# Optimization experiments

Measured on AMD Instinct MI355X. Metric: run time of the kernel, lower is better.

Reference implementation:

```python
import jax, jax.numpy as jnp
import numpy as np

N_EMBED = 1024
N_HEAD = 16
EPS = 1.1920929e-07  # torch.finfo(float32).eps, nn.RMSNorm default eps=None


def rmsnorm(x, w):
    var = jnp.mean(x * x, axis=-1, keepdims=True)
    return x * jax.lax.rsqrt(var + EPS) * w


def setup_inputs() -> dict:
    key = jax.random.key(0)
    ks = jax.random.split(key, 12)
    d = N_EMBED
    s = lambda fan_in: 1.0 / np.sqrt(fan_in)
    inp = {
        "x": jax.random.normal(ks[0], (2, 2048, d), jnp.float32),
        "w_attn": jax.random.uniform(ks[1], (d, 3 * d), jnp.float32, -s(d), s(d)),
        "b_attn": jax.random.uniform(ks[2], (3 * d,), jnp.float32, -s(d), s(d)),
        "w_proj": jax.random.uniform(ks[3], (d, d), jnp.float32, -s(d), s(d)),
        "b_proj": jax.random.uniform(ks[4], (d,), jnp.float32, -s(d), s(d)),
        "w_fc1": jax.random.uniform(ks[5], (d, 4 * d), jnp.float32, -s(d), s(d)),
        "b_fc1": jax.random.uniform(ks[6], (4 * d,), jnp.float32, -s(d), s(d)),
        "w_fc2": jax.random.uniform(ks[7], (4 * d, d), jnp.float32, -s(4 * d), s(4 * d)),
        "b_fc2": jax.random.uniform(ks[8], (d,), jnp.float32, -s(4 * d), s(4 * d)),
        "g_norm1": jnp.ones((d,), jnp.float32),
        "g_norm2": jnp.ones((d,), jnp.float32),
    }
    return inp


def reference(x, w_attn, b_attn, w_proj, b_proj, w_fc1, b_fc1, w_fc2, b_fc2, g_norm1, g_norm2):
    B, T, d = x.shape
    H = N_HEAD
    hd = d // H

    # --- attention branch ---
    h = rmsnorm(x, g_norm1)
    qkv = h @ w_attn + b_attn  # [B,T,3d]
    q, k, v = jnp.split(qkv, 3, axis=-1)
    q = q.reshape(B, T, H, hd).transpose(0, 2, 1, 3)  # [B,H,T,hd]
    k = k.reshape(B, T, H, hd).transpose(0, 2, 1, 3)
    v = v.reshape(B, T, H, hd).transpose(0, 2, 1, 3)
    qk = jnp.einsum('bhqd,bhkd->bhqk', q, k)  # NOTE: no logit scaling (as in source)
    mask = jnp.tril(jnp.ones((T, T), bool))
    qk = jnp.where(mask, qk, -jnp.inf)
    # source scales softmax OUTPUT by n_embed**-0.5 (faithful quirk)
    attn = jax.nn.softmax(qk, axis=-1) * (d ** -0.5)
    o = jnp.einsum('bhqk,bhkd->bhqd', attn, v)
    o = o.transpose(0, 2, 1, 3).reshape(B, T, d)
    x = x + (o @ w_proj + b_proj)

    # --- MLP branch ---
    h = rmsnorm(x, g_norm2)
    h = jax.nn.gelu(h @ w_fc1 + b_fc1, approximate=False)
    x = x + (h @ w_fc2 + b_fc2)
    return x
```

## Files before the change

kernel.cpp:

```cpp
#include <hip/hip_runtime.h>
#include <hip/hip_bf16.h>


typedef __hip_bfloat16 bf16;
typedef __attribute__((ext_vector_type(8))) short short8;
typedef __attribute__((ext_vector_type(4))) float floatx4;

__device__ __forceinline__ float bits2f(unsigned short u) {
  union { unsigned int i; float f; } c; c.i = ((unsigned int)u) << 16; return c.f;
}
__device__ __forceinline__ unsigned short f2bits(float f) {
  bf16 b = __float2bfloat16(f);
  union { bf16 b; unsigned short u; } c; c.b = b; return c.u;
}

__device__ __forceinline__ void gld_lds16(const unsigned short* g, unsigned short* l) {
  __builtin_amdgcn_global_load_lds(
      (const __attribute__((address_space(1))) void*)g,
      (__attribute__((address_space(3))) void*)l, 16, 0, 0);
}

__global__ __launch_bounds__(256) void rmsnorm_r10(const float* __restrict__ x,
                                                   const float* __restrict__ g,
                                                   unsigned short* __restrict__ out)
{
  const int row = blockIdx.x, tid = threadIdx.x;
  const size_t rb = (size_t)row * 1024;
  float4 xv = *(const float4*)(x + rb + tid * 4);
  float v[4] = {xv.x, xv.y, xv.z, xv.w};
  float s = v[0]*v[0] + v[1]*v[1] + v[2]*v[2] + v[3]*v[3];
  #pragma unroll
  for (int off = 32; off > 0; off >>= 1) s += __shfl_down(s, off, 64);
  __shared__ float part[4];
  if ((tid & 63) == 0) part[tid >> 6] = s;
  __syncthreads();
  const float tot = part[0] + part[1] + part[2] + part[3];
  const float sc = rsqrtf(tot * (1.0f / 1024.0f) + 1.1920929e-07f);
  float4 gv = *(const float4*)(g + tid * 4);
  ushort4 o4 = { f2bits(v[0] * sc * gv.x), f2bits(v[1] * sc * gv.y),
                 f2bits(v[2] * sc * gv.z), f2bits(v[3] * sc * gv.w) };
  *(ushort4*)(out + rb + tid * 4) = o4;
}

__global__ __launch_bounds__(256) void wprep_r10(const float* __restrict__ in,
                                                 unsigned short* __restrict__ out,
                                                 int K, int N)
{
  __shared__ unsigned short tile[32][33];
  const int tid = threadIdx.x;
  const int k0 = blockIdx.y * 32, n0 = blockIdx.x * 32;
  const int tr = tid >> 3, tc4 = (tid & 7) * 4;
  float4 v = *(const float4*)(in + (size_t)(k0 + tr) * N + n0 + tc4);
  tile[tr][tc4 + 0] = f2bits(v.x);
  tile[tr][tc4 + 1] = f2bits(v.y);
  tile[tr][tc4 + 2] = f2bits(v.z);
  tile[tr][tc4 + 3] = f2bits(v.w);
  __syncthreads();
  ushort4 o = { tile[tc4 + 0][tr], tile[tc4 + 1][tr],
                tile[tc4 + 2][tr], tile[tc4 + 3][tr] };
  *(ushort4*)(out + (size_t)(n0 + tr) * K + k0 + tc4) = o;
}

template<int EPI>
__global__ __launch_bounds__(256) void gemm_r10(
    const unsigned short* __restrict__ A,
    const unsigned short* __restrict__ BT,
    const float* __restrict__ bias,
    const float* __restrict__ resid,
    void* __restrict__ Cout,
    int M, int N, int K, int Klen)
{
  __shared__ __align__(16) unsigned short As[2][128 * 32];
  __shared__ __align__(16) unsigned short Bs[2][128 * 32];
  const int tid = threadIdx.x;
  const int lane = tid & 63;
  const int wv = tid >> 6;
  const int m0 = blockIdx.y * 128, n0 = blockIdx.x * 128;
  const int wm = (wv >> 1) * 64, wn = (wv & 1) * 64;
  const int kbase = blockIdx.z * Klen;

  const int s0 = tid, s1 = tid + 256;
  const int r0 = s0 >> 2, kq0 = (s0 & 3) ^ ((r0 >> 1) & 3);
  const int r1 = s1 >> 2, kq1 = (s1 & 3) ^ ((r1 >> 1) & 3);
  const unsigned short* Ab = A  + (size_t)m0 * K;
  const unsigned short* Bb = BT + (size_t)n0 * K;
  const size_t ga0 = (size_t)r0 * K + kq0 * 8 + kbase;
  const size_t ga1 = (size_t)r1 * K + kq1 * 8 + kbase;

  floatx4 acc[4][4];
  #pragma unroll
  for (int i = 0; i < 4; ++i)
    #pragma unroll
    for (int j = 0; j < 4; ++j)
      acc[i][j] = (floatx4){0.f, 0.f, 0.f, 0.f};

  int aoff[4], boff[4];
  #pragma unroll
  for (int i = 0; i < 4; ++i) {
    int ra = wm + i * 16 + (lane & 15);
    aoff[i] = (ra * 4 + ((lane >> 4) ^ ((ra >> 1) & 3))) * 8;
    int rb = wn + i * 16 + (lane & 15);
    boff[i] = (rb * 4 + ((lane >> 4) ^ ((rb >> 1) & 3))) * 8;
  }

  gld_lds16(Ab + ga0, As[0] + s0 * 8);
  gld_lds16(Ab + ga1, As[0] + s1 * 8);
  gld_lds16(Bb + ga0, Bs[0] + s0 * 8);
  gld_lds16(Bb + ga1, Bs[0] + s1 * 8);
  __syncthreads();

  const int nsteps = Klen >> 5;
  for (int t = 0; t < nsteps; ++t) {
    const int cur = t & 1;
    if (t + 1 < nsteps) {
      const size_t ko = (size_t)(t + 1) * 32;
      gld_lds16(Ab + ga0 + ko, As[cur ^ 1] + s0 * 8);
      gld_lds16(Ab + ga1 + ko, As[cur ^ 1] + s1 * 8);
      gld_lds16(Bb + ga0 + ko, Bs[cur ^ 1] + s0 * 8);
      gld_lds16(Bb + ga1 + ko, Bs[cur ^ 1] + s1 * 8);
    }

    short8 af[4], bfr[4];
    #pragma unroll
    for (int i = 0; i < 4; ++i) {
      af[i]  = *(const short8*)(As[cur] + aoff[i]);
      bfr[i] = *(const short8*)(Bs[cur] + boff[i]);
    }
    #pragma unroll
    for (int i = 0; i < 4; ++i)
      #pragma unroll
      for (int j = 0; j < 4; ++j)
        acc[i][j] = __builtin_amdgcn_mfma_f32_16x16x32_bf16(af[i], bfr[j], acc[i][j], 0, 0, 0);

    __syncthreads();
  }

  float* Cp32 = (float*)Cout;
  if constexpr (EPI == 4) Cp32 += (size_t)blockIdx.z * ((size_t)M * N);

  #pragma unroll
  for (int i = 0; i < 4; ++i) {
    #pragma unroll
    for (int j = 0; j < 4; ++j) {
      const int rbase = m0 + wm + i * 16 + (lane >> 4) * 4;
      const int c = n0 + wn + j * 16 + (lane & 15);
      float bia = 0.0f;
      if constexpr (EPI != 4) bia = bias[c];
      #pragma unroll
      for (int r = 0; r < 4; ++r) {
        float v = acc[i][j][r] + bia;
        const size_t idx = (size_t)(rbase + r) * N + c;
        if constexpr (EPI == 0) {
          ((unsigned short*)Cout)[idx] = f2bits(v);
        } else if constexpr (EPI == 1) {
          ((float*)Cout)[idx] = v + resid[idx];
        } else if constexpr (EPI == 2) {
          v = 0.5f * v * (1.0f + erff(v * 0.70710678118654752f));
          ((unsigned short*)Cout)[idx] = f2bits(v);
        } else if constexpr (EPI == 3) {
          ((float*)Cout)[idx] = v + resid[idx];
        } else {
          Cp32[idx] = v;
        }
      }
    }
  }
}

__global__ __launch_bounds__(256) void red2_r10(const float* __restrict__ P,
                                                const float* __restrict__ resid,
                                                const float* __restrict__ bias,
                                                float* __restrict__ out)
{
  const size_t i = ((size_t)blockIdx.x * 256 + threadIdx.x) * 4;
  const int col = (int)(i & 1023);
  float4 p0 = *(const float4*)(P + i);
  float4 p1 = *(const float4*)(P + ((size_t)4096 * 1024) + i);
  float4 xr = *(const float4*)(resid + i);
  float4 b  = *(const float4*)(bias + col);
  float4 o  = { p0.x + p1.x + xr.x + b.x, p0.y + p1.y + xr.y + b.y,
                p0.z + p1.z + xr.z + b.z, p0.w + p1.w + xr.w + b.w };
  *(float4*)(out + i) = o;
}

__global__ __launch_bounds__(512) void attn_r10(const unsigned short* __restrict__ qkv,
                                                unsigned short* __restrict__ o)
{
  __shared__ __align__(16) unsigned short Qs[128 * 64];
  __shared__ __align__(16) unsigned short Ks[2][64 * 64];
  __shared__ __align__(16) unsigned short VT[2][64 * 72];
  __shared__ __align__(16) unsigned short Ps[128 * 72];
  __shared__ __align__(16) float stat_s[128];

  const int tid = threadIdx.x, lane = tid & 63, wv = tid >> 6;
  const int quad = lane >> 4, l15 = lane & 15;
  const int qt0 = blockIdx.x, bh = blockIdx.y;
  const int b = bh >> 4, h = bh & 15;
  const size_t base = (size_t)b * 2048 * 3072;
  const int qcol = h * 64, kcol = 1024 + h * 64, vcol = 2048 + h * 64;

  const int sr = tid >> 3, scp = tid & 7, sc = scp ^ (sr & 7);
  const unsigned short* kgp = qkv + base + (size_t)sr * 3072 + kcol + sc * 8;
  const int vp = tid & 31, vdc = tid >> 5;
  const unsigned short* vgp = qkv + base + (size_t)(2 * vp) * 3072 + vcol + vdc * 4;

  for (int pass = 0; pass < 2; ++pass) {
    const int qt = pass ? qt0 : 15 - qt0;
    const int q0 = qt * 128;
    const int nkt = 2 * qt + 2;

    __syncthreads();

    #pragma unroll
    for (int p = 0; p < 2; ++p) {
      int s = tid + 512 * p;
      int r = s >> 3, cp = s & 7, c = cp ^ (r & 7);
      gld_lds16(qkv + base + (size_t)(q0 + r) * 3072 + qcol + c * 8, Qs + s * 8);
    }
    gld_lds16(kgp, Ks[0] + tid * 8);
    {
      uint2 u0 = *(const uint2*)vgp;
      uint2 u1 = *(const uint2*)(vgp + 3072);
      unsigned short* dst = VT[0] + (size_t)(vdc * 4) * 72 + 2 * vp;
      *(unsigned int*)(dst + 0 * 72) = (u0.x & 0xffffu) | (u1.x << 16);
      *(unsigned int*)(dst + 1 * 72) = (u0.x >> 16)     | (u1.x & 0xffff0000u);
      *(unsigned int*)(dst + 2 * 72) = (u0.y & 0xffffu) | (u1.y << 16);
      *(unsigned int*)(dst + 3 * 72) = (u0.y >> 16)     | (u1.y & 0xffff0000u);
    }
    __syncthreads();

    short8 qa[2];
    #pragma unroll
    for (int ks = 0; ks < 2; ++ks) {
      int ra = wv * 16 + l15;
      int cp = (ks * 4 + quad) ^ (ra & 7);
      qa[ks] = *(const short8*)(Qs + (ra * 8 + cp) * 8);
    }

    floatx4 oacc[4];
    #pragma unroll
    for (int dt = 0; dt < 4; ++dt) oacc[dt] = (floatx4){0.f, 0.f, 0.f, 0.f};
    float m_i[4], l_i[4];
    #pragma unroll
    for (int r = 0; r < 4; ++r) { m_i[r] = -3.0e38f; l_i[r] = 0.0f; }

    for (int kt = 0; kt < nkt; ++kt) {
      const int cur = kt & 1;
      const bool pf = (kt + 1 < nkt);
      uint2 u0, u1;
      if (pf) {
        const size_t koff = (size_t)(kt + 1) * 64 * 3072;
        gld_lds16(kgp + koff, Ks[cur ^ 1] + tid * 8);
        u0 = *(const uint2*)(vgp + koff);
        u1 = *(const uint2*)(vgp + koff + 3072);
      }

      short8 kb[4][2];
      #pragma unroll
      for (int j = 0; j < 4; ++j)
        #pragma unroll
        for (int ks = 0; ks < 2; ++ks) {
          int rb = j * 16 + l15;
          int cp = (ks * 4 + quad) ^ (rb & 7);
          kb[j][ks] = *(const short8*)(Ks[cur] + (rb * 8 + cp) * 8);
        }
      floatx4 s_[4];
      #pragma unroll
      for (int j = 0; j < 4; ++j) s_[j] = (floatx4){0.f, 0.f, 0.f, 0.f};
      #pragma unroll
      for (int j = 0; j < 4; ++j)
        #pragma unroll
        for (int ks = 0; ks < 2; ++ks)
          s_[j] = __builtin_amdgcn_mfma_f32_16x16x32_bf16(qa[ks], kb[j][ks], s_[j], 0, 0, 0);

      const int k0 = kt * 64;
      const int rowmin = q0 + wv * 16;
      const int rowb = rowmin + quad * 4;
      if (k0 + 63 > rowmin) {
        #pragma unroll
        for (int j = 0; j < 4; ++j) {
          const int col = k0 + j * 16 + l15;
          #pragma unroll
          for (int r = 0; r < 4; ++r)
            if (col > rowb + r) s_[j][r] = -3.0e38f;
        }
      }
      float fm[4], al[4], rs[4];
      #pragma unroll
      for (int r = 0; r < 4; ++r)
        fm[r] = fmaxf(fmaxf(s_[0][r], s_[1][r]), fmaxf(s_[2][r], s_[3][r]));
      #pragma unroll
      for (int msk = 1; msk < 16; msk <<= 1)
        #pragma unroll
        for (int r = 0; r < 4; ++r)
          fm[r] = fmaxf(fm[r], __shfl_xor(fm[r], msk, 64));
      #pragma unroll
      for (int r = 0; r < 4; ++r) {
        const float mn = fmaxf(m_i[r], fm[r]);
        al[r] = __expf(m_i[r] - mn);
        m_i[r] = mn;
      }
      #pragma unroll
      for (int j = 0; j < 4; ++j)
        #pragma unroll
        for (int r = 0; r < 4; ++r)
          s_[j][r] = __expf(s_[j][r] - m_i[r]);
      #pragma unroll
      for (int r = 0; r < 4; ++r)
        rs[r] = (s_[0][r] + s_[1][r]) + (s_[2][r] + s_[3][r]);
      #pragma unroll
      for (int msk = 1; msk < 16; msk <<= 1)
        #pragma unroll
        for (int r = 0; r < 4; ++r)
          rs[r] += __shfl_xor(rs[r], msk, 64);
      #pragma unroll
      for (int r = 0; r < 4; ++r)
        l_i[r] = l_i[r] * al[r] + rs[r];
      if (l15 == 0) {
        float4 a4 = { al[0], al[1], al[2], al[3] };
        *(float4*)(stat_s + wv * 16 + quad * 4) = a4;
      }
      #pragma unroll
      for (int j = 0; j < 4; ++j)
        #pragma unroll
        for (int r = 0; r < 4; ++r)
          Ps[(size_t)(wv * 16 + quad * 4 + r) * 72 + j * 16 + l15] = f2bits(s_[j][r]);

      const float alq = stat_s[wv * 16 + l15];
      #pragma unroll
      for (int dt = 0; dt < 4; ++dt)
        #pragma unroll
        for (int r = 0; r < 4; ++r)
          oacc[dt][r] *= alq;

      short8 va[4][2], pb[2];
      #pragma unroll
      for (int dt = 0; dt < 4; ++dt)
        #pragma unroll
        for (int ks = 0; ks < 2; ++ks)
          va[dt][ks] = *(const short8*)(VT[cur] + (size_t)(dt * 16 + l15) * 72 + ks * 32 + quad * 8);
      #pragma unroll
      for (int ks = 0; ks < 2; ++ks)
        pb[ks] = *(const short8*)(Ps + (size_t)(wv * 16 + l15) * 72 + ks * 32 + quad * 8);
      #pragma unroll
      for (int dt = 0; dt < 4; ++dt)
        #pragma unroll
        for (int ks = 0; ks < 2; ++ks)
          oacc[dt] = __builtin_amdgcn_mfma_f32_16x16x32_bf16(va[dt][ks], pb[ks], oacc[dt], 0, 0, 0);

      if (pf) {
        unsigned short* dst = VT[cur ^ 1] + (size_t)(vdc * 4) * 72 + 2 * vp;
        *(unsigned int*)(dst + 0 * 72) = (u0.x & 0xffffu) | (u1.x << 16);
        *(unsigned int*)(dst + 1 * 72) = (u0.x >> 16)     | (u1.x & 0xffff0000u);
        *(unsigned int*)(dst + 2 * 72) = (u0.y & 0xffffu) | (u1.y << 16);
        *(unsigned int*)(dst + 3 * 72) = (u0.y >> 16)     | (u1.y & 0xffff0000u);
      }
      __syncthreads();
    }

    if (l15 == 0) {
      float4 l4 = { l_i[0], l_i[1], l_i[2], l_i[3] };
      *(float4*)(stat_s + wv * 16 + quad * 4) = l4;
    }
    const float linv = 0.03125f / stat_s[wv * 16 + l15];
    const size_t row = (size_t)b * 2048 + q0 + wv * 16 + l15;
    #pragma unroll
    for (int dt = 0; dt < 4; ++dt) {
      const int col = h * 64 + dt * 16 + quad * 4;
      ushort4 o4 = { f2bits(oacc[dt][0] * linv), f2bits(oacc[dt][1] * linv),
                     f2bits(oacc[dt][2] * linv), f2bits(oacc[dt][3] * linv) };
      *(ushort4*)(o + row * 1024 + col) = o4;
    }
  }
}

extern "C" void kernel_launch(void* const* d_in, const int* in_sizes, int n_in,
                              void* d_out, int out_size, void* d_ws, size_t ws_size,
                              hipStream_t stream)
{
  (void)in_sizes; (void)n_in; (void)out_size; (void)ws_size;
  const float* x      = (const float*)d_in[0];
  const float* w_attn = (const float*)d_in[1];
  const float* b_attn = (const float*)d_in[2];
  const float* w_proj = (const float*)d_in[3];
  const float* b_proj = (const float*)d_in[4];
  const float* w_fc1  = (const float*)d_in[5];
  const float* b_fc1  = (const float*)d_in[6];
  const float* w_fc2  = (const float*)d_in[7];
  const float* b_fc2  = (const float*)d_in[8];
  const float* g1     = (const float*)d_in[9];
  const float* g2     = (const float*)d_in[10];
  float* out = (float*)d_out;

  char* ws = (char*)d_ws;
  unsigned short* h   = (unsigned short*)(ws);
  unsigned short* qkv = (unsigned short*)(ws + ((size_t)8  << 20));
  unsigned short* ov  = (unsigned short*)(ws);
  float*          x1  = (float*)         (ws + ((size_t)32 << 20));
  unsigned short* h2  = (unsigned short*)(ws + ((size_t)8  << 20));
  unsigned short* h3  = (unsigned short*)(ws + ((size_t)48 << 20));
  unsigned short* WT  = (unsigned short*)(ws + ((size_t)80 << 20));
  float*          P   = (float*)(ws);

  const int M = 4096;

  rmsnorm_r10<<<M, 256, 0, stream>>>(x, g1, h);
  wprep_r10<<<dim3(3072 / 32, 1024 / 32), 256, 0, stream>>>(w_attn, WT, 1024, 3072);
  gemm_r10<0><<<dim3(3072 / 128, M / 128), 256, 0, stream>>>(h, WT, b_attn, nullptr, qkv, M, 3072, 1024, 1024);
  attn_r10<<<dim3(8, 32), 512, 0, stream>>>(qkv, ov);
  wprep_r10<<<dim3(1024 / 32, 1024 / 32), 256, 0, stream>>>(w_proj, WT, 1024, 1024);
  gemm_r10<1><<<dim3(1024 / 128, M / 128), 256, 0, stream>>>(ov, WT, b_proj, x, x1, M, 1024, 1024, 1024);
  rmsnorm_r10<<<M, 256, 0, stream>>>(x1, g2, h2);
  wprep_r10<<<dim3(4096 / 32, 1024 / 32), 256, 0, stream>>>(w_fc1, WT, 1024, 4096);
  gemm_r10<2><<<dim3(4096 / 128, M / 128), 256, 0, stream>>>(h2, WT, b_fc1, nullptr, h3, M, 4096, 1024, 1024);
  wprep_r10<<<dim3(1024 / 32, 4096 / 32), 256, 0, stream>>>(w_fc2, WT, 4096, 1024);
  gemm_r10<4><<<dim3(1024 / 128, M / 128, 2), 256, 0, stream>>>(h3, WT, nullptr, nullptr, P, M, 1024, 4096, 2048);
  red2_r10<<<4096, 256, 0, stream>>>(P, x1, b_fc2, out);
}
```

Before: 386.5 us.

## Add 256x256-tile GEMM with 4-stage LDS pipeline for QKV and FC1

Adds a new GEMM kernel that uses 512 threads, 256x256 output tiles, and a 4-buffer LDS ring that prefetches two K-steps ahead. The QKV and FC1 projections now use it instead of the 128x128 kernel. Larger tiles raise arithmetic intensity and reduce global traffic per FLOP, and the deeper prefetch hides load latency. In exchange, the block count drops: QKV gets 192 blocks and FC1 gets 256 on a 256-CU device, so wave quantization and lower occupancy from 64KB+ of LDS are risks.

```diff
diff --git a/kernel.cpp b/kernel.cpp
--- a/kernel.cpp
+++ b/kernel.cpp
@@ -20,7 +20,7 @@
       (__attribute__((address_space(3))) void*)l, 16, 0, 0);
 }
 
-__global__ __launch_bounds__(256) void rmsnorm_r10(const float* __restrict__ x,
+__global__ __launch_bounds__(256) void rmsnorm_r15(const float* __restrict__ x,
                                                    const float* __restrict__ g,
                                                    unsigned short* __restrict__ out)
 {
@@ -42,7 +42,7 @@
   *(ushort4*)(out + rb + tid * 4) = o4;
 }
 
-__global__ __launch_bounds__(256) void wprep_r10(const float* __restrict__ in,
+__global__ __launch_bounds__(256) void wprep_r15(const float* __restrict__ in,
                                                  unsigned short* __restrict__ out,
                                                  int K, int N)
 {
@@ -62,7 +62,7 @@
 }
 
 template<int EPI>
-__global__ __launch_bounds__(256) void gemm_r10(
+__global__ __launch_bounds__(256) void gemm128_r15(
     const unsigned short* __restrict__ A,
     const unsigned short* __restrict__ BT,
     const float* __restrict__ bias,
@@ -167,7 +167,112 @@
   }
 }
 
-__global__ __launch_bounds__(256) void red2_r10(const float* __restrict__ P,
+template<int EPI>
+__global__ __launch_bounds__(512) void gemm256_r15(
+    const unsigned short* __restrict__ A,
+    const unsigned short* __restrict__ BT,
+    const float* __restrict__ bias,
+    void* __restrict__ Cout,
+    int M, int N, int K)
+{
+  __shared__ __align__(16) unsigned short As[4][256 * 32];
+  __shared__ __align__(16) unsigned short Bs[4][256 * 32];
+  const int tid = threadIdx.x;
+  const int lane = tid & 63, wv = tid >> 6;
+  const int quad = lane >> 4, l15 = lane & 15;
+  const int m0 = blockIdx.y * 256, n0 = blockIdx.x * 256;
+  const int wm = (wv >> 2) * 128, wn = (wv & 3) * 64;
+
+  const int s0 = tid, s1 = tid + 512;
+  const int r0 = s0 >> 2, kq0 = (s0 & 3) ^ ((r0 >> 1) & 3);
+  const int r1 = s1 >> 2, kq1 = (s1 & 3) ^ ((r1 >> 1) & 3);
+  const unsigned short* Ab = A  + (size_t)m0 * K;
+  const unsigned short* Bb = BT + (size_t)n0 * K;
+  const size_t ga0 = (size_t)r0 * K + kq0 * 8;
+  const size_t ga1 = (size_t)r1 * K + kq1 * 8;
+
+  floatx4 acc[8][4];
+  #pragma unroll
+  for (int i = 0; i < 8; ++i)
+    #pragma unroll
+    for (int j = 0; j < 4; ++j)
+      acc[i][j] = (floatx4){0.f, 0.f, 0.f, 0.f};
+
+  int aoff[8], boff[4];
+  #pragma unroll
+  for (int i = 0; i < 8; ++i) {
+    int ra = wm + i * 16 + l15;
+    aoff[i] = (ra * 4 + (quad ^ ((ra >> 1) & 3))) * 8;
+  }
+  #pragma unroll
+  for (int j = 0; j < 4; ++j) {
+    int rb = wn + j * 16 + l15;
+    boff[j] = (rb * 4 + (quad ^ ((rb >> 1) & 3))) * 8;
+  }
+
+  #define STG_R15(t) { const size_t ko = (size_t)(t) * 32; const int bb = (t) & 3; \
+    gld_lds16(Ab + ga0 + ko, As[bb] + s0 * 8); \
+    gld_lds16(Ab + ga1 + ko, As[bb] + s1 * 8); \
+    gld_lds16(Bb + ga0 + ko, Bs[bb] + s0 * 8); \
+    gld_lds16(Bb + ga1 + ko, Bs[bb] + s1 * 8); }
+
+  STG_R15(0);
+  STG_R15(1);
+
+  const int nsteps = K >> 5;
+  for (int t = 0; t < nsteps; ++t) {
+    const int cur = t & 3;
+    if (t + 2 < nsteps) {
+      STG_R15(t + 2);
+      asm volatile("s_waitcnt vmcnt(8)" ::: "memory");
+    } else if (t + 1 < nsteps) {
+      asm volatile("s_waitcnt vmcnt(4)" ::: "memory");
+    } else {
+      asm volatile("s_waitcnt vmcnt(0)" ::: "memory");
+    }
+    __builtin_amdgcn_s_barrier();
+    asm volatile("" ::: "memory");
+
+    short8 bfr[4];
+    #pragma unroll
+    for (int j = 0; j < 4; ++j)
+      bfr[j] = *(const short8*)(Bs[cur] + boff[j]);
+    #pragma unroll
+    for (int ih = 0; ih < 2; ++ih) {
+      short8 af[4];
+      #pragma unroll
+      for (int k = 0; k < 4; ++k)
+        af[k] = *(const short8*)(As[cur] + aoff[ih * 4 + k]);
+      #pragma unroll
+      for (int k = 0; k < 4; ++k)
+        #pragma unroll
+        for (int j = 0; j < 4; ++j)
+          acc[ih * 4 + k][j] = __builtin_amdgcn_mfma_f32_16x16x32_bf16(af[k], bfr[j], acc[ih * 4 + k][j], 0, 0, 0);
+    }
+  }
+  #undef STG_R15
+
+  #pragma unroll
+  for (int i = 0; i < 8; ++i) {
+    #pragma unroll
+    for (int j = 0; j < 4; ++j) {
+      const int rbase = m0 + wm + i * 16 + quad * 4;
+      const int c = n0 + wn + j * 16 + l15;
+      const float bia = bias[c];
+      #pragma unroll
+      for (int r = 0; r < 4; ++r) {
+        float v = acc[i][j][r] + bia;
+        const size_t idx = (size_t)(rbase + r) * N + c;
+        if constexpr (EPI == 2) {
+          v = 0.5f * v * (1.0f + erff(v * 0.70710678118654752f));
+        }
+        ((unsigned short*)Cout)[idx] = f2bits(v);
+      }
+    }
+  }
+}
+
+__global__ __launch_bounds__(256) void red2_r15(const float* __restrict__ P,
                                                 const float* __restrict__ resid,
                                                 const float* __restrict__ bias,
                                                 float* __restrict__ out)
@@ -183,7 +288,7 @@
   *(float4*)(out + i) = o;
 }
 
-__global__ __launch_bounds__(512) void attn_r10(const unsigned short* __restrict__ qkv,
+__global__ __launch_bounds__(512) void attn_r15(const unsigned short* __restrict__ qkv,
                                                 unsigned short* __restrict__ o)
 {
   __shared__ __align__(16) unsigned short Qs[128 * 64];
@@ -404,16 +509,16 @@
 
   const int M = 4096;
 
-  rmsnorm_r10<<<M, 256, 0, stream>>>(x, g1, h);
-  wprep_r10<<<dim3(3072 / 32, 1024 / 32), 256, 0, stream>>>(w_attn, WT, 1024, 3072);
-  gemm_r10<0><<<dim3(3072 / 128, M / 128), 256, 0, stream>>>(h, WT, b_attn, nullptr, qkv, M, 3072, 1024, 1024);
-  attn_r10<<<dim3(8, 32), 512, 0, stream>>>(qkv, ov);
-  wprep_r10<<<dim3(1024 / 32, 1024 / 32), 256, 0, stream>>>(w_proj, WT, 1024, 1024);
-  gemm_r10<1><<<dim3(1024 / 128, M / 128), 256, 0, stream>>>(ov, WT, b_proj, x, x1, M, 1024, 1024, 1024);
-  rmsnorm_r10<<<M, 256, 0, stream>>>(x1, g2, h2);
-  wprep_r10<<<dim3(4096 / 32, 1024 / 32), 256, 0, stream>>>(w_fc1, WT, 1024, 4096);
-  gemm_r10<2><<<dim3(4096 / 128, M / 128), 256, 0, stream>>>(h2, WT, b_fc1, nullptr, h3, M, 4096, 1024, 1024);
-  wprep_r10<<<dim3(1024 / 32, 4096 / 32), 256, 0, stream>>>(w_fc2, WT, 4096, 1024);
-  gemm_r10<4><<<dim3(1024 / 128, M / 128, 2), 256, 0, stream>>>(h3, WT, nullptr, nullptr, P, M, 1024, 4096, 2048);
-  red2_r10<<<4096, 256, 0, stream>>>(P, x1, b_fc2, out);
-}
+  rmsnorm_r15<<<M, 256, 0, stream>>>(x, g1, h);
+  wprep_r15<<<dim3(3072 / 32, 1024 / 32), 256, 0, stream>>>(w_attn, WT, 1024, 3072);
+  gemm256_r15<0><<<dim3(3072 / 256, M / 256), 512, 0, stream>>>(h, WT, b_attn, qkv, M, 3072, 1024);
+  attn_r15<<<dim3(8, 32), 512, 0, stream>>>(qkv, ov);
+  wprep_r15<<<dim3(1024 / 32, 1024 / 32), 256, 0, stream>>>(w_proj, WT, 1024, 1024);
+  gemm128_r15<1><<<dim3(1024 / 128, M / 128), 256, 0, stream>>>(ov, WT, b_proj, x, x1, M, 1024, 1024, 1024);
+  rmsnorm_r15<<<M, 256, 0, stream>>>(x1, g2, h2);
+  wprep_r15<<<dim3(4096 / 32, 1024 / 32), 256, 0, stream>>>(w_fc1, WT, 1024, 4096);
+  gemm256_r15<2><<<dim3(4096 / 256, M / 256), 512, 0, stream>>>(h2, WT, b_fc1, h3, M, 4096, 1024);
+  wprep_r15<<<dim3(1024 / 32, 4096 / 32), 256, 0, stream>>>(w_fc2, WT, 4096, 1024);
+  gemm128_r15<4><<<dim3(1024 / 128, M / 128, 2), 256, 0, stream>>>(h3, WT, nullptr, nullptr, P, M, 1024, 4096, 2048);
+  red2_r15<<<4096, 256, 0, stream>>>(P, x1, b_fc2, out);
+}
```

Result: no change. 379.4 us (-1.8%).
